# Performance work log

Hardware: AMD Instinct MI355X
Metric: run time of the kernel (lower is better)

The kernel has to match this reference:

```python
import jax, jax.numpy as jnp
import numpy as np

B, N, T, H, P = 512, 128, 336, 32, 1  # batch, nodes, seq_len, hidden, pred_len


def setup_inputs() -> dict:
    key = jax.random.key(0)
    ks = jax.random.split(key, 9)
    s = 1.0 / np.sqrt(H)  # torch LSTM/Linear init bound
    u = lambda k, shape: jax.random.uniform(k, shape, dtype=jnp.float32, minval=-s, maxval=s)
    return {
        "x": jax.random.normal(ks[0], (B, N, T), dtype=jnp.float32),
        # layer 0: input_size=1
        "W_ih0": u(ks[1], (N, 4 * H, 1)),
        "W_hh0": u(ks[2], (N, 4 * H, H)),
        "b0": u(ks[3], (N, 4 * H)),  # = b_ih0 + b_hh0 (additive in the cell)
        # layer 1: input_size=H
        "W_ih1": u(ks[4], (N, 4 * H, H)),
        "W_hh1": u(ks[5], (N, 4 * H, H)),
        "b1": u(ks[6], (N, 4 * H)),
        # per-node linear head
        "W_fc": u(ks[7], (N, P, H)),
        "b_fc": u(ks[8], (N, P)),
    }


def _cell(x_proj, h, c, W_hh, b):
    # x_proj, h, c: [B, N, H*(...)]; torch gate order: i, f, g, o
    gates = x_proj + jnp.einsum("bnh,ngh->bng", h, W_hh) + b
    i, f, g, o = jnp.split(gates, 4, axis=-1)
    c = jax.nn.sigmoid(f) * c + jax.nn.sigmoid(i) * jnp.tanh(g)
    h = jax.nn.sigmoid(o) * jnp.tanh(c)
    return h, c


def reference(x, W_ih0, W_hh0, b0, W_ih1, W_hh1, b1, W_fc, b_fc):
    Bx, Nx, Tx = x.shape
    Hx = W_hh0.shape[-1]
    Wi0 = W_ih0[:, :, 0]  # [N, 4H] since input_size == 1
    xs = jnp.moveaxis(x, 2, 0)  # [T, B, N]
    zeros = jnp.zeros((Bx, Nx, Hx), x.dtype)
    init = (zeros, zeros, zeros, zeros)  # h0, c0, h1, c1

    def step(carry, x_t):
        h0, c0, h1, c1 = carry
        xp0 = x_t[:, :, None] * Wi0[None]          # [B, N, 4H]
        h0, c0 = _cell(xp0, h0, c0, W_hh0, b0)
        xp1 = jnp.einsum("bnh,ngh->bng", h0, W_ih1)
        h1, c1 = _cell(xp1, h1, c1, W_hh1, b1)
        return (h0, c0, h1, c1), None

    (h0, c0, h1, c1), _ = jax.lax.scan(step, init, xs)
    # last-timestep top-layer hidden through per-node linear head
    return jnp.einsum("bnh,nph->bnp", h1, W_fc) + b_fc[None]
```

## Files before the change

kernel.cpp:

```cpp
#include <hip/hip_runtime.h>
#include <stdint.h>

#define NB 512
#define NN 128
#define NT 336
#define NH 32
#define NG 128

typedef short bf16x8 __attribute__((ext_vector_type(8)));
typedef float f32x4  __attribute__((ext_vector_type(4)));
typedef float f32x2  __attribute__((ext_vector_type(2)));
typedef float f32v4  __attribute__((ext_vector_type(4)));

#define LOG2E 1.4426950408889634f
#define KNEG  (-2.0f * LOG2E)

__device__ __forceinline__ f32x2 exp2v(f32x2 v) {
  f32x2 r; r.x = __builtin_amdgcn_exp2f(v.x); r.y = __builtin_amdgcn_exp2f(v.y); return r;
}
__device__ __forceinline__ f32x2 rcpv(f32x2 v) {
  f32x2 r; r.x = __builtin_amdgcn_rcpf(v.x); r.y = __builtin_amdgcn_rcpf(v.y); return r;
}
__device__ __forceinline__ short f2bf(float f) {
  unsigned u = __builtin_bit_cast(unsigned, f) + 0x8000u;
  return (short)(u >> 16);
}

template<bool BIAS>
__device__ __forceinline__ f32x2 cell_pair(f32x2 gi, f32x2 gf, f32x2 gg, f32x2 go,
                                           f32x2& cst, float ebi, float ebf,
                                           float ebg, float kng, float ebo) {
  f32x2 wi = exp2v(gi), wf = exp2v(gf), uu = exp2v(gg), wo = exp2v(go);
  f32x2 Ai, Af, Au, Ao, nuk;
  if (BIAS) {
    Ai  = wi * ebi + 1.0f;
    Af  = wf * ebf + 1.0f;
    Au  = uu * ebg + 1.0f;
    Ao  = wo * ebo + 1.0f;
    nuk = uu * kng + KNEG;
  } else {
    Ai  = wi + 1.0f; Af = wf + 1.0f; Au = uu + 1.0f; Ao = wo + 1.0f;
    nuk = uu * (-KNEG) + KNEG;
  }
  f32x2 P  = Ai * Au;
  f32x2 N  = cst * P + nuk * Af;
  f32x2 cS = N * rcpv(Af * P);
  cst = cS;
  f32x2 sarg = cS;
  sarg.x = fminf(sarg.x, 80.0f);
  sarg.y = fminf(sarg.y, 80.0f);
  f32x2 vv = exp2v(sarg);
  f32x2 hh = (1.0f - vv) * rcpv(Ao * (vv + 1.0f));
  return hh;
}

#define WSTRIDE 40
#define HSTRIDE 32
__global__ __launch_bounds__(256, 3) void lstm_kernel(
    const float* __restrict__ x,
    const float* __restrict__ Wih0,
    const float* __restrict__ Whh0,
    const float* __restrict__ b0,
    const float* __restrict__ Wih1,
    const float* __restrict__ Whh1,
    const float* __restrict__ b1,
    const float* __restrict__ Wfc,
    const float* __restrict__ bfc,
    float* __restrict__ out)
{
  const int tid  = threadIdx.x;
  const int wave = tid >> 6;
  const int lane = tid & 63;
  const int c    = lane & 15;
  const int q    = lane >> 4;
  const int n    = blockIdx.x >> 3;
  const int m0   = ((blockIdx.x & 7) * 4 + wave) * 16;

  __shared__ short lds_w[3 * NG * WSTRIDE];
  __shared__ short lds_h[4 * 2 * 16 * HSTRIDE];
  short* my0 = lds_h + wave * (2 * 16 * HSTRIDE);
  short* my1 = my0 + 16 * HSTRIDE;

  {
    const float* srcs[3] = { Whh0 + n * (NG * NH), Wih1 + n * (NG * NH),
                             Whh1 + n * (NG * NH) };
#pragma unroll 1
    for (int idx = tid; idx < 3 * NG * NH; idx += 256) {
      int mat = idx >> 12;
      int rem = idx & 4095;
      int row = rem >> 5, col = rem & 31;
      float sc = (row >= 64 && row < 96) ? (-2.0f * LOG2E) : (-LOG2E);
      lds_w[mat * (NG * WSTRIDE) + row * WSTRIDE + col] = f2bf(sc * srcs[mat][rem]);
    }
  }

  float b0g[8], eb1[8], wi0g[8];
#pragma unroll
  for (int tau = 0; tau < 8; ++tau) {
    int g = tau * 16 + c;
    float sc = (tau == 4 || tau == 5) ? (-2.0f * LOG2E) : (-LOG2E);
    b0g[tau]  = sc * b0[n * NG + g];
    eb1[tau]  = __builtin_amdgcn_exp2f(sc * b1[n * NG + g]);
    wi0g[tau] = sc * Wih0[n * NG + g];
  }
  const float kng4 = (-KNEG) * eb1[4];
  const float kng5 = (-KNEG) * eb1[5];
  const float wfc0 = Wfc[n * NH + c];
  const float wfc1 = Wfc[n * NH + 16 + c];

  __syncthreads();

  const short* wbase = lds_w + c * WSTRIDE + q * 8;

  const float* px0 = x + ((size_t)(m0 + q * 4 + 0) * NN + n) * NT;
  const float* px1 = x + ((size_t)(m0 + q * 4 + 1) * NN + n) * NT;
  const float* px2 = x + ((size_t)(m0 + q * 4 + 2) * NN + n) * NT;
  const float* px3 = x + ((size_t)(m0 + q * 4 + 3) * NN + n) * NT;

  bf16x8 a0 = {0,0,0,0,0,0,0,0};
  bf16x8 a1 = {0,0,0,0,0,0,0,0};
  f32x2 c0p[2][2], c1p[2][2];
#pragma unroll
  for (int tu = 0; tu < 2; ++tu)
#pragma unroll
    for (int p = 0; p < 2; ++p) {
      c0p[tu][p] = (f32x2){0.f, 0.f};
      c1p[tu][p] = (f32x2){0.f, 0.f};
    }

  const f32x4 zero4 = {0.f, 0.f, 0.f, 0.f};

#pragma unroll 1
  for (int t4 = 0; t4 < NT / 4; ++t4) {
    f32v4 xr0 = *(const f32v4*)(px0 + t4 * 4);
    f32v4 xr1 = *(const f32v4*)(px1 + t4 * 4);
    f32v4 xr2 = *(const f32v4*)(px2 + t4 * 4);
    f32v4 xr3 = *(const f32v4*)(px3 + t4 * 4);

#pragma unroll
    for (int ts = 0; ts < 4; ++ts) {
      f32x2 x01 = {xr0[ts], xr1[ts]};
      f32x2 x23 = {xr2[ts], xr3[ts]};

#pragma unroll
      for (int tu = 0; tu < 2; ++tu) {
        f32x4 acc[4];
#pragma unroll
        for (int k = 0; k < 4; ++k) {
          int tau = tu + 2 * k;
          f32x2 w2 = {wi0g[tau], wi0g[tau]};
          f32x2 b2 = {b0g[tau], b0g[tau]};
          f32x2 lo = x01 * w2 + b2;
          f32x2 hi = x23 * w2 + b2;
          acc[k] = (f32x4){lo.x, lo.y, hi.x, hi.y};
        }
#pragma unroll
        for (int k = 0; k < 4; ++k) {
          int tau = tu + 2 * k;
          bf16x8 bw = *(const bf16x8*)(wbase + 0 * (NG * WSTRIDE) + tau * (16 * WSTRIDE));
          acc[k] = __builtin_amdgcn_mfma_f32_16x16x32_bf16(a0, bw, acc[k], 0, 0, 0);
        }
#pragma unroll
        for (int p = 0; p < 2; ++p) {
          f32x2 gi = { acc[0][2*p], acc[0][2*p+1] };
          f32x2 gf = { acc[1][2*p], acc[1][2*p+1] };
          f32x2 gg = { acc[2][2*p], acc[2][2*p+1] };
          f32x2 go = { acc[3][2*p], acc[3][2*p+1] };
          f32x2 hh = cell_pair<false>(gi, gf, gg, go, c0p[tu][p],
                                      1.f, 1.f, 1.f, 1.f, 1.f);
          my0[(q * 4 + 2*p    ) * HSTRIDE + tu * 16 + c] = f2bf(hh.x);
          my0[(q * 4 + 2*p + 1) * HSTRIDE + tu * 16 + c] = f2bf(hh.y);
        }
      }
      asm volatile("" ::: "memory");
      a0 = *(const bf16x8*)(my0 + c * HSTRIDE + q * 8);

#pragma unroll
      for (int tu = 0; tu < 2; ++tu) {
        f32x4 acc[4];
#pragma unroll
        for (int k = 0; k < 4; ++k) {
          int tau = tu + 2 * k;
          bf16x8 b1f = *(const bf16x8*)(wbase + 1 * (NG * WSTRIDE) + tau * (16 * WSTRIDE));
          acc[k] = __builtin_amdgcn_mfma_f32_16x16x32_bf16(a0, b1f, zero4, 0, 0, 0);
        }
#pragma unroll
        for (int k = 0; k < 4; ++k) {
          int tau = tu + 2 * k;
          bf16x8 b2f = *(const bf16x8*)(wbase + 2 * (NG * WSTRIDE) + tau * (16 * WSTRIDE));
          acc[k] = __builtin_amdgcn_mfma_f32_16x16x32_bf16(a1, b2f, acc[k], 0, 0, 0);
        }
#pragma unroll
        for (int p = 0; p < 2; ++p) {
          f32x2 gi = { acc[0][2*p], acc[0][2*p+1] };
          f32x2 gf = { acc[1][2*p], acc[1][2*p+1] };
          f32x2 gg = { acc[2][2*p], acc[2][2*p+1] };
          f32x2 go = { acc[3][2*p], acc[3][2*p+1] };
          f32x2 hh = cell_pair<true>(gi, gf, gg, go, c1p[tu][p],
                                     eb1[tu], eb1[tu + 2], eb1[tu + 4],
                                     (tu == 0) ? kng4 : kng5, eb1[tu + 6]);
          my1[(q * 4 + 2*p    ) * HSTRIDE + tu * 16 + c] = f2bf(hh.x);
          my1[(q * 4 + 2*p + 1) * HSTRIDE + tu * 16 + c] = f2bf(hh.y);
        }
      }
      asm volatile("" ::: "memory");
      a1 = *(const bf16x8*)(my1 + c * HSTRIDE + q * 8);
    }
  }

  float h1v[2][4];
#pragma unroll
  for (int tu = 0; tu < 2; ++tu)
#pragma unroll
    for (int r = 0; r < 4; ++r) {
      unsigned short us = (unsigned short)my1[(q * 4 + r) * HSTRIDE + tu * 16 + c];
      h1v[tu][r] = __builtin_bit_cast(float, ((unsigned)us) << 16);
    }
  float s0 = h1v[0][0] * wfc0 + h1v[1][0] * wfc1;
  float s1 = h1v[0][1] * wfc0 + h1v[1][1] * wfc1;
  float s2 = h1v[0][2] * wfc0 + h1v[1][2] * wfc1;
  float s3 = h1v[0][3] * wfc0 + h1v[1][3] * wfc1;
#pragma unroll
  for (int off = 1; off < 16; off <<= 1) {
    s0 += __shfl_xor(s0, off, 64);
    s1 += __shfl_xor(s1, off, 64);
    s2 += __shfl_xor(s2, off, 64);
    s3 += __shfl_xor(s3, off, 64);
  }
  if (c < 4) {
    float v = (c == 0) ? s0 : (c == 1) ? s1 : (c == 2) ? s2 : s3;
    out[(size_t)(m0 + q * 4 + c) * NN + n] = v + bfc[n];
  }
}

extern "C" void kernel_launch(void* const* d_in, const int* in_sizes, int n_in,
                              void* d_out, int out_size, void* d_ws, size_t ws_size,
                              hipStream_t stream) {
  const float* x    = (const float*)d_in[0];
  const float* Wih0 = (const float*)d_in[1];
  const float* Whh0 = (const float*)d_in[2];
  const float* b0   = (const float*)d_in[3];
  const float* Wih1 = (const float*)d_in[4];
  const float* Whh1 = (const float*)d_in[5];
  const float* b1   = (const float*)d_in[6];
  const float* Wfc  = (const float*)d_in[7];
  const float* bfc  = (const float*)d_in[8];
  float* out = (float*)d_out;

  lstm_kernel<<<dim3(1024), dim3(256), 0, stream>>>(
      x, Wih0, Whh0, b0, Wih1, Whh1, b1, Wfc, bfc, out);
}
```

Before: 1.318 ms.

## Keep W_hh1 fragments in registers and store other weights fragment-major in LDS

The layer-1 recurrent weight fragments are now loaded once into per-lane bf16x8 registers instead of being read from LDS on every timestep. The remaining two weight matrices are stored in LDS in a lane-contiguous fragment order, so each lane reads its 16-byte fragment with unit stride and no row padding. LDS use shrinks and the occupancy hint rises from 3 to 4 blocks per SM. The extra 32 VGPRs for the register weights may conflict with the higher occupancy target and could cause spills.

```diff
diff --git a/kernel.cpp b/kernel.cpp
--- a/kernel.cpp
+++ b/kernel.cpp
@@ -54,9 +54,8 @@
   return hh;
 }
 
-#define WSTRIDE 40
 #define HSTRIDE 32
-__global__ __launch_bounds__(256, 3) void lstm_kernel(
+__global__ __launch_bounds__(256, 4) void lstm_kernel(
     const float* __restrict__ x,
     const float* __restrict__ Wih0,
     const float* __restrict__ Whh0,
@@ -76,21 +75,38 @@
   const int n    = blockIdx.x >> 3;
   const int m0   = ((blockIdx.x & 7) * 4 + wave) * 16;
 
-  __shared__ short lds_w[3 * NG * WSTRIDE];
+  __shared__ short lds_w[2 * 8 * 64 * 8];
   __shared__ short lds_h[4 * 2 * 16 * HSTRIDE];
   short* my0 = lds_h + wave * (2 * 16 * HSTRIDE);
   short* my1 = my0 + 16 * HSTRIDE;
 
   {
-    const float* srcs[3] = { Whh0 + n * (NG * NH), Wih1 + n * (NG * NH),
-                             Whh1 + n * (NG * NH) };
+    const float* srcs[2] = { Whh0 + n * (NG * NH), Wih1 + n * (NG * NH) };
 #pragma unroll 1
-    for (int idx = tid; idx < 3 * NG * NH; idx += 256) {
-      int mat = idx >> 12;
-      int rem = idx & 4095;
-      int row = rem >> 5, col = rem & 31;
-      float sc = (row >= 64 && row < 96) ? (-2.0f * LOG2E) : (-LOG2E);
-      lds_w[mat * (NG * WSTRIDE) + row * WSTRIDE + col] = f2bf(sc * srcs[mat][rem]);
+    for (int idx = tid; idx < 2 * 8 * 64; idx += 256) {
+      int mat = idx >> 9;
+      int rem = idx & 511;
+      int tau = rem >> 6;
+      int ln  = rem & 63;
+      int cc  = ln & 15, qq = ln >> 4;
+      float sc = (tau == 4 || tau == 5) ? (-2.0f * LOG2E) : (-LOG2E);
+      const float* src = srcs[mat] + (tau * 16 + cc) * NH + qq * 8;
+      bf16x8 frag;
+#pragma unroll
+      for (int j = 0; j < 8; ++j) frag[j] = f2bf(sc * src[j]);
+      *(bf16x8*)(lds_w + idx * 8) = frag;
+    }
+  }
+
+  bf16x8 wb2[8];
+  {
+    const float* pW2 = Whh1 + n * (NG * NH);
+#pragma unroll
+    for (int tau = 0; tau < 8; ++tau) {
+      int off = (tau * 16 + c) * NH + q * 8;
+      float sc = (tau == 4 || tau == 5) ? (-2.0f * LOG2E) : (-LOG2E);
+#pragma unroll
+      for (int j = 0; j < 8; ++j) wb2[tau][j] = f2bf(sc * pW2[off + j]);
     }
   }
 
@@ -110,7 +126,7 @@
 
   __syncthreads();
 
-  const short* wbase = lds_w + c * WSTRIDE + q * 8;
+  const short* wfrag = lds_w + lane * 8;
 
   const float* px0 = x + ((size_t)(m0 + q * 4 + 0) * NN + n) * NT;
   const float* px1 = x + ((size_t)(m0 + q * 4 + 1) * NN + n) * NT;
@@ -157,7 +173,7 @@
 #pragma unroll
         for (int k = 0; k < 4; ++k) {
           int tau = tu + 2 * k;
-          bf16x8 bw = *(const bf16x8*)(wbase + 0 * (NG * WSTRIDE) + tau * (16 * WSTRIDE));
+          bf16x8 bw = *(const bf16x8*)(wfrag + (0 * 8 + tau) * 512);
           acc[k] = __builtin_amdgcn_mfma_f32_16x16x32_bf16(a0, bw, acc[k], 0, 0, 0);
         }
 #pragma unroll
@@ -181,14 +197,13 @@
 #pragma unroll
         for (int k = 0; k < 4; ++k) {
           int tau = tu + 2 * k;
-          bf16x8 b1f = *(const bf16x8*)(wbase + 1 * (NG * WSTRIDE) + tau * (16 * WSTRIDE));
+          bf16x8 b1f = *(const bf16x8*)(wfrag + (1 * 8 + tau) * 512);
           acc[k] = __builtin_amdgcn_mfma_f32_16x16x32_bf16(a0, b1f, zero4, 0, 0, 0);
         }
 #pragma unroll
         for (int k = 0; k < 4; ++k) {
           int tau = tu + 2 * k;
-          bf16x8 b2f = *(const bf16x8*)(wbase + 2 * (NG * WSTRIDE) + tau * (16 * WSTRIDE));
-          acc[k] = __builtin_amdgcn_mfma_f32_16x16x32_bf16(a1, b2f, acc[k], 0, 0, 0);
+          acc[k] = __builtin_amdgcn_mfma_f32_16x16x32_bf16(a1, wb2[tau], acc[k], 0, 0, 0);
         }
 #pragma unroll
         for (int p = 0; p < 2; ++p) {
```

Measured after the change: 2.392 ms. 81.5% more time.
